# Optimization experiments

Measured on AMD Instinct MI355X. Metric: run time of the kernel, lower is better.

Reference implementation:

```python
import jax, jax.numpy as jnp
import numpy as np


def _make_cameras(key, B):
    """Well-conditioned c = [cam2world(16), intrinsics(9)] per batch."""
    k1, k2 = jax.random.split(key)
    # random rotation via Gram-Schmidt on a random 3x3
    A = jax.random.normal(k1, (B, 3, 3), dtype=jnp.float32)
    q0 = A[:, :, 0] / jnp.linalg.norm(A[:, :, 0], axis=-1, keepdims=True)
    v1 = A[:, :, 1] - jnp.sum(A[:, :, 1] * q0, -1, keepdims=True) * q0
    q1 = v1 / jnp.linalg.norm(v1, axis=-1, keepdims=True)
    q2 = jnp.cross(q0, q1)
    R = jnp.stack([q0, q1, q2], axis=-1)                      # [B,3,3]
    t = 2.7 * q2                                              # camera at radius 2.7 along view axis
    cam2world = jnp.zeros((B, 4, 4), jnp.float32)
    cam2world = cam2world.at[:, :3, :3].set(R)
    cam2world = cam2world.at[:, :3, 3].set(t)
    cam2world = cam2world.at[:, 3, 3].set(1.0)
    # EG3D-style normalized intrinsics: fx=fy=4.2647, cx=cy=0.5, sk=0
    intr = jnp.tile(jnp.array([[4.2647, 0.0, 0.5],
                               [0.0, 4.2647, 0.5],
                               [0.0, 0.0, 1.0]], jnp.float32), (B, 1, 1))
    return jnp.concatenate([cam2world.reshape(B, 16), intr.reshape(B, 9)], axis=1)


def setup_inputs() -> dict:
    key = jax.random.key(0)
    kc, kd, kp = jax.random.split(key, 3)
    B, R, M = 8, 64, 4096
    c = _make_cameras(kc, B)
    image_depth = 2.2 + 1.1 * jax.random.uniform(kd, (B, R * R, 1), dtype=jnp.float32)
    pc = 0.3 * jax.random.normal(kp, (B, M, 3), dtype=jnp.float32)
    return {"c": c, "image_depth": image_depth, "pc": pc, "resolution": R}


def _ray_sampler(cam2world, intrinsics, resolution):
    B = cam2world.shape[0]
    N = resolution * resolution
    fx = intrinsics[:, 0, 0][:, None]
    fy = intrinsics[:, 1, 1][:, None]
    cx = intrinsics[:, 0, 2][:, None]
    cy = intrinsics[:, 1, 2][:, None]
    sk = intrinsics[:, 0, 1][:, None]
    r = (jnp.arange(resolution, dtype=jnp.float32) + 0.5) / resolution
    gi, gj = jnp.meshgrid(r, r, indexing='ij')                # row, col
    x_cam = jnp.broadcast_to(gj.reshape(-1), (B, N))          # uv.flip(0): x is col coord
    y_cam = jnp.broadcast_to(gi.reshape(-1), (B, N))
    z_cam = jnp.ones((B, N), jnp.float32)
    x_lift = (x_cam - cx + cy * sk / fy - sk * y_cam / fy) / fx * z_cam
    y_lift = (y_cam - cy) / fy * z_cam
    cam_rel = jnp.stack([x_lift, y_lift, z_cam, jnp.ones_like(z_cam)], axis=-1)  # [B,N,4]
    world = jnp.einsum('bij,bnj->bni', cam2world, cam_rel)[..., :3]
    origins = cam2world[:, :3, 3]                              # [B,3]
    dirs = world - origins[:, None, :]
    dirs = dirs / jnp.linalg.norm(dirs, axis=-1, keepdims=True)
    ray_origins = jnp.broadcast_to(origins[:, None, :], dirs.shape)
    return ray_origins, dirs


def _chamfer(x, y):
    # squared-distance NN both directions; GEMM-form pairwise distances
    x2 = jnp.sum(x * x, axis=-1)                               # [B,N]
    y2 = jnp.sum(y * y, axis=-1)                               # [B,M]
    xy = jnp.einsum('bnd,bmd->bnm', x, y)                      # [B,N,M]
    d = x2[:, :, None] + y2[:, None, :] - 2.0 * xy
    return jnp.min(d, axis=2), jnp.min(d, axis=1)              # dist1 [B,N], dist2 [B,M]


def reference(c, image_depth, pc, resolution):
    B = c.shape[0]
    pc = pc[..., :3]
    depth = image_depth.reshape(B, -1, 1)
    cam2world = c[:, :16].reshape(-1, 4, 4)
    intr = c[:, 16:25].reshape(-1, 3, 3)
    ro, rd = _ray_sampler(cam2world, intr, resolution)
    pred_pos = depth * rd + ro                                  # [B,N,3]
    d0, d1 = _chamfer(pred_pos, pc)
    K = min(pred_pos.shape[1], pc.shape[1]) // 2
    d0s = jnp.sort(d0, axis=1)[:, :K]
    d1s = d0s  # NOTE: faithful to original code (loss_1_sorted is assigned from loss_0_sorted)
    loss0 = jnp.mean(d0s, axis=1)
    loss1 = jnp.mean(d1s, axis=1)
    return (loss0 + loss1).reshape(B, 1)
```

## Files before the change

### kernel.cpp

```cpp
#include <hip/hip_runtime.h>
#include <math.h>

#define FLT_BIG 3.0e38f
#define HIST_BINS 16384

typedef short short8 __attribute__((ext_vector_type(8)));
typedef float floatx16 __attribute__((ext_vector_type(16)));

union U4S8 { uint4 u; short8 s; };

static __device__ __forceinline__ unsigned int f2bf(float f) {
    unsigned int u = __float_as_uint(f);
    return (u + 0x7FFFu + ((u >> 16) & 1u)) >> 16;
}
static __device__ __forceinline__ float bf2f(unsigned int b) {
    return __uint_as_float(b << 16);
}

__global__ __launch_bounds__(256) void pack_frags_kernel(
    const float* __restrict__ pc,
    uint4* __restrict__ frags,
    int total)
{
    const int idx = blockIdx.x * 256 + threadIdx.x;
    if (idx >= total) return;
    const float x = pc[idx * 3 + 0];
    const float y = pc[idx * 3 + 1];
    const float z = pc[idx * 3 + 2];
    const float hq = 0.5f * (x * x + y * y + z * z);
    uint4 u;
    u.x = f2bf(x) | (f2bf(y) << 16);
    u.y = f2bf(z) | (f2bf(hq) << 16);
    u.z = 0x3F803F80u;
    u.w = 0u;
    frags[idx] = u;
}

__global__ __launch_bounds__(256, 4) void chamfer_mfma_kernel(
    const float* __restrict__ cparam,
    const float* __restrict__ depth,
    const uint4* __restrict__ frags,
    float* __restrict__ d0,
    int N, int M, int R)
{
    const int b    = blockIdx.y;
    const int tid  = threadIdx.x;
    const int lane = tid & 63;
    const int wv   = tid >> 6;
    const int row  = lane & 31;
    const int half = lane >> 5;

    __shared__ float smin[4][32];

    const float* cb = cparam + (size_t)b * 25;
    const float fx = cb[16], sk = cb[17], cx = cb[18];
    const float fy = cb[20], cy = cb[21];

    const int nbase = blockIdx.x * 32;
    const int n  = nbase + row;
    const int i0 = n / R;
    const int j0 = n - i0 * R;
    const float x_cam = (j0 + 0.5f) / (float)R;
    const float y_cam = (i0 + 0.5f) / (float)R;
    const float x_lift = (x_cam - cx + cy * sk / fy - sk * y_cam / fy) / fx;
    const float y_lift = (y_cam - cy) / fy;
    const float dxw = cb[0] * x_lift + cb[1] * y_lift + cb[2];
    const float dyw = cb[4] * x_lift + cb[5] * y_lift + cb[6];
    const float dzw = cb[8] * x_lift + cb[9] * y_lift + cb[10];
    const float inv = 1.0f / sqrtf(dxw * dxw + dyw * dyw + dzw * dzw);
    const float dep = depth[(size_t)b * N + n];
    const float px = cb[3]  + dep * dxw * inv;
    const float py = cb[7]  + dep * dyw * inv;
    const float pz = cb[11] + dep * dzw * inv;

    const float hp = 0.5f * (px * px + py * py + pz * pz);
    const unsigned int hp_hi = f2bf(hp);
    const unsigned int hp_lo = f2bf(hp - bf2f(hp_hi));

    U4S8 af;
    af.u = make_uint4(0u, 0u, 0u, 0u);
    if (half == 0) {
        af.u.x = f2bf(-px) | (f2bf(-py) << 16);
        af.u.y = f2bf(-pz) | (0x3F80u << 16);
        af.u.z = hp_hi | (hp_lo << 16);
    }
    const short8 afrag = af.s;
    const floatx16 zero16 = {0,0,0,0,0,0,0,0,0,0,0,0,0,0,0,0};

    float minsA[16], minsB[16];
    #pragma unroll
    for (int t = 0; t < 16; t++) { minsA[t] = FLT_BIG; minsB[t] = FLT_BIG; }

    const uint4* fb = frags + (size_t)b * M + (wv << 10);
    for (int f = 0; f < 32; f += 8) {
        uint4 bu[8];
        #pragma unroll
        for (int mm = 0; mm < 8; mm++)
            bu[mm] = fb[((f + mm) << 5) + row];
        #pragma unroll
        for (int mm = 0; mm < 8; mm++) {
            U4S8 bf; bf.u = bu[mm];
            floatx16 d = __builtin_amdgcn_mfma_f32_32x32x16_bf16(
                             afrag, bf.s, zero16, 0, 0, 0);
            if (mm & 1) {
                #pragma unroll
                for (int t = 0; t < 16; t++) minsB[t] = fminf(minsB[t], d[t]);
            } else {
                #pragma unroll
                for (int t = 0; t < 16; t++) minsA[t] = fminf(minsA[t], d[t]);
            }
        }
    }

    #pragma unroll
    for (int t = 0; t < 16; t++) {
        float v = fminf(minsA[t], minsB[t]);
        v = fminf(v, __shfl_xor(v, 1));
        v = fminf(v, __shfl_xor(v, 2));
        v = fminf(v, __shfl_xor(v, 4));
        v = fminf(v, __shfl_xor(v, 8));
        v = fminf(v, __shfl_xor(v, 16));
        minsA[t] = v;
    }
    if (row == 0) {
        #pragma unroll
        for (int t = 0; t < 16; t++)
            smin[wv][(t & 3) + 8 * (t >> 2) + 4 * half] = minsA[t];
    }
    __syncthreads();

    if (tid < 32) {
        const float v = fminf(fminf(smin[0][tid], smin[1][tid]),
                              fminf(smin[2][tid], smin[3][tid]));
        d0[(size_t)b * N + nbase + tid] = fmaxf(2.0f * v, 0.0f);
    }
}

__global__ __launch_bounds__(256, 1) void select_mean_kernel(
    const float* __restrict__ d0,
    float* __restrict__ out,
    int N, int K)
{
    const int b   = blockIdx.x;
    const int tid = threadIdx.x;

    extern __shared__ unsigned int hist[];
    __shared__ unsigned int spart[256];
    __shared__ unsigned int s_selbin, s_krem;
    __shared__ unsigned int subcnt[32];
    __shared__ float        subsum[32];
    __shared__ float        s_below;

    for (int t2 = tid; t2 < HIST_BINS; t2 += 256) hist[t2] = 0u;
    if (tid < 32) { subcnt[tid] = 0u; subsum[tid] = 0.0f; }
    if (tid == 0) s_below = 0.0f;
    __syncthreads();

    unsigned int key[16];
    #pragma unroll
    for (int t2 = 0; t2 < 16; t2++)
        key[t2] = __float_as_uint(d0[(size_t)b * N + t2 * 256 + tid]);
    #pragma unroll
    for (int t2 = 0; t2 < 16; t2++)
        atomicAdd(&hist[key[t2] >> 18], 1u);
    __syncthreads();

    unsigned int psum = 0u;
    #pragma unroll 8
    for (int i2 = 0; i2 < 64; i2++)
        psum += hist[(tid << 6) + ((i2 + tid) & 63)];
    spart[tid] = psum;
    __syncthreads();

    unsigned int cbef = 0u;
    for (int i2 = 0; i2 < tid; i2++) cbef += spart[i2];
    if (cbef < (unsigned int)K && (unsigned int)K <= cbef + psum) {
        unsigned int k2 = (unsigned int)K - cbef;
        unsigned int sel = 0u;
        for (int i2 = 0; i2 < 64; i2++) {
            unsigned int h = hist[(tid << 6) + i2];
            if (k2 <= h) { sel = (tid << 6) + i2; break; }
            k2 -= h;
        }
        s_selbin = sel;
        s_krem   = k2;
    }
    __syncthreads();

    const unsigned int selbin = s_selbin;
    float sumb = 0.0f;
    #pragma unroll
    for (int t2 = 0; t2 < 16; t2++) {
        const unsigned int bin = key[t2] >> 18;
        const float v = __uint_as_float(key[t2]);
        if (bin < selbin) sumb += v;
        if (bin == selbin) {
            const unsigned int sub = (key[t2] >> 13) & 31u;
            atomicAdd(&subcnt[sub], 1u);
            atomicAdd(&subsum[sub], v);
        }
    }
    atomicAdd(&s_below, sumb);
    __syncthreads();

    if (tid == 0) {
        unsigned int k2 = s_krem;
        float s = s_below;
        for (int i2 = 0; i2 < 32; i2++) {
            unsigned int h = subcnt[i2];
            if (k2 <= h) {
                s += (h ? (subsum[i2] * ((float)k2 / (float)h)) : 0.0f);
                break;
            }
            s += subsum[i2];
            k2 -= h;
        }
        out[b] = 2.0f * s / (float)K;
    }
}

extern "C" void kernel_launch(void* const* d_in, const int* in_sizes, int n_in,
                              void* d_out, int out_size, void* d_ws, size_t ws_size,
                              hipStream_t stream)
{
    const float* c   = (const float*)d_in[0];
    const float* dep = (const float*)d_in[1];
    const float* pc  = (const float*)d_in[2];
    float* out = (float*)d_out;

    const int B = in_sizes[0] / 25;
    const int N = in_sizes[1] / B;
    const int M = in_sizes[2] / (3 * B);
    int R = 1; while (R * R < N) R++;
    const int K = ((N < M) ? N : M) / 2;

    float* d0    = (float*)d_ws;
    uint4* frags = (uint4*)((char*)d_ws + (size_t)B * N * sizeof(float));

    const int total = B * M;
    hipLaunchKernelGGL(pack_frags_kernel, dim3((total + 255) / 256), dim3(256),
                       0, stream, pc, frags, total);

    dim3 gridA(N / 32, B);
    hipLaunchKernelGGL(chamfer_mfma_kernel, gridA, dim3(256), 0, stream,
                       c, dep, frags, d0, N, M, R);

    size_t ldsB = (size_t)HIST_BINS * sizeof(unsigned int);
    hipLaunchKernelGGL(select_mean_kernel, dim3(B), dim3(256), ldsB, stream,
                       d0, out, N, K);
}
```

Before: 82.62 us.

## Fuse point packing into chamfer kernel and widen select kernel to 1024 threads

Removes the separate pack kernel: the chamfer kernel now reads raw fp32 point coordinates and builds the bf16 MFMA B fragments in-register, including the half squared norm. The select/mean kernel moves to 1024 threads per batch, replacing the serial per-thread prefix loop over 256 partials with wave-level shuffle scans and a shuffle-reduced below-sum. This saves one launch and a round-trip through workspace. In exchange, every block now repacks every point (repeated conversion ALU work across N/32 blocks) and issues strided 12-byte loads in place of 16-byte vector loads.

```diff
diff --git a/kernel.cpp b/kernel.cpp
--- a/kernel.cpp
+++ b/kernel.cpp
@@ -17,29 +17,10 @@
     return __uint_as_float(b << 16);
 }
 
-__global__ __launch_bounds__(256) void pack_frags_kernel(
-    const float* __restrict__ pc,
-    uint4* __restrict__ frags,
-    int total)
-{
-    const int idx = blockIdx.x * 256 + threadIdx.x;
-    if (idx >= total) return;
-    const float x = pc[idx * 3 + 0];
-    const float y = pc[idx * 3 + 1];
-    const float z = pc[idx * 3 + 2];
-    const float hq = 0.5f * (x * x + y * y + z * z);
-    uint4 u;
-    u.x = f2bf(x) | (f2bf(y) << 16);
-    u.y = f2bf(z) | (f2bf(hq) << 16);
-    u.z = 0x3F803F80u;
-    u.w = 0u;
-    frags[idx] = u;
-}
-
 __global__ __launch_bounds__(256, 4) void chamfer_mfma_kernel(
     const float* __restrict__ cparam,
     const float* __restrict__ depth,
-    const uint4* __restrict__ frags,
+    const float* __restrict__ pc,
     float* __restrict__ d0,
     int N, int M, int R)
 {
@@ -91,15 +72,25 @@
     #pragma unroll
     for (int t = 0; t < 16; t++) { minsA[t] = FLT_BIG; minsB[t] = FLT_BIG; }
 
-    const uint4* fb = frags + (size_t)b * M + (wv << 10);
+    const float* qb = pc + ((size_t)b * M + ((size_t)wv << 10)) * 3;
     for (int f = 0; f < 32; f += 8) {
-        uint4 bu[8];
-        #pragma unroll
-        for (int mm = 0; mm < 8; mm++)
-            bu[mm] = fb[((f + mm) << 5) + row];
+        float qx[8], qy[8], qz[8];
         #pragma unroll
         for (int mm = 0; mm < 8; mm++) {
-            U4S8 bf; bf.u = bu[mm];
+            const int p = (((f + mm) << 5) + row) * 3;
+            qx[mm] = qb[p + 0];
+            qy[mm] = qb[p + 1];
+            qz[mm] = qb[p + 2];
+        }
+        #pragma unroll
+        for (int mm = 0; mm < 8; mm++) {
+            const float x = qx[mm], y = qy[mm], z = qz[mm];
+            const float hq = 0.5f * (x * x + y * y + z * z);
+            U4S8 bf;
+            bf.u.x = f2bf(x) | (f2bf(y) << 16);
+            bf.u.y = f2bf(z) | (f2bf(hq) << 16);
+            bf.u.z = 0x3F803F80u;
+            bf.u.w = 0u;
             floatx16 d = __builtin_amdgcn_mfma_f32_32x32x16_bf16(
                              afrag, bf.s, zero16, 0, 0, 0);
             if (mm & 1) {
@@ -136,50 +127,70 @@
     }
 }
 
-__global__ __launch_bounds__(256, 1) void select_mean_kernel(
+__global__ __launch_bounds__(1024, 1) void select_mean_kernel(
     const float* __restrict__ d0,
     float* __restrict__ out,
     int N, int K)
 {
-    const int b   = blockIdx.x;
-    const int tid = threadIdx.x;
+    const int b    = blockIdx.x;
+    const int tid  = threadIdx.x;
+    const int lane = tid & 63;
+    const int w    = tid >> 6;
 
     extern __shared__ unsigned int hist[];
-    __shared__ unsigned int spart[256];
+    __shared__ unsigned int wsums[16];
     __shared__ unsigned int s_selbin, s_krem;
     __shared__ unsigned int subcnt[32];
     __shared__ float        subsum[32];
     __shared__ float        s_below;
 
-    for (int t2 = tid; t2 < HIST_BINS; t2 += 256) hist[t2] = 0u;
+    #pragma unroll
+    for (int i = 0; i < 16; i++) hist[(i << 10) + tid] = 0u;
     if (tid < 32) { subcnt[tid] = 0u; subsum[tid] = 0.0f; }
     if (tid == 0) s_below = 0.0f;
     __syncthreads();
 
-    unsigned int key[16];
-    #pragma unroll
-    for (int t2 = 0; t2 < 16; t2++)
-        key[t2] = __float_as_uint(d0[(size_t)b * N + t2 * 256 + tid]);
-    #pragma unroll
-    for (int t2 = 0; t2 < 16; t2++)
-        atomicAdd(&hist[key[t2] >> 18], 1u);
+    unsigned int key[4];
+    #pragma unroll
+    for (int t = 0; t < 4; t++)
+        key[t] = __float_as_uint(d0[(size_t)b * N + (t << 10) + tid]);
+    #pragma unroll
+    for (int t = 0; t < 4; t++)
+        atomicAdd(&hist[key[t] >> 18], 1u);
     __syncthreads();
 
     unsigned int psum = 0u;
-    #pragma unroll 8
-    for (int i2 = 0; i2 < 64; i2++)
-        psum += hist[(tid << 6) + ((i2 + tid) & 63)];
-    spart[tid] = psum;
-    __syncthreads();
-
-    unsigned int cbef = 0u;
-    for (int i2 = 0; i2 < tid; i2++) cbef += spart[i2];
+    #pragma unroll
+    for (int i = 0; i < 16; i++)
+        psum += hist[(tid << 4) + ((i + tid) & 15)];
+
+    unsigned int inc = psum;
+    #pragma unroll
+    for (int dd = 1; dd < 64; dd <<= 1) {
+        unsigned int y = __shfl_up(inc, dd);
+        if (lane >= dd) inc += y;
+    }
+    if (lane == 63) wsums[w] = inc;
+    __syncthreads();
+    if (tid < 16) {
+        const unsigned int v = wsums[tid];
+        unsigned int in2 = v;
+        #pragma unroll
+        for (int dd = 1; dd < 16; dd <<= 1) {
+            unsigned int y = __shfl_up(in2, dd);
+            if ((int)tid >= dd) in2 += y;
+        }
+        wsums[tid] = in2 - v;
+    }
+    __syncthreads();
+    const unsigned int cbef = wsums[w] + (inc - psum);
+
     if (cbef < (unsigned int)K && (unsigned int)K <= cbef + psum) {
         unsigned int k2 = (unsigned int)K - cbef;
         unsigned int sel = 0u;
-        for (int i2 = 0; i2 < 64; i2++) {
-            unsigned int h = hist[(tid << 6) + i2];
-            if (k2 <= h) { sel = (tid << 6) + i2; break; }
+        for (int i = 0; i < 16; i++) {
+            unsigned int h = hist[(tid << 4) + i];
+            if (k2 <= h) { sel = (tid << 4) + i; break; }
             k2 -= h;
         }
         s_selbin = sel;
@@ -190,17 +201,19 @@
     const unsigned int selbin = s_selbin;
     float sumb = 0.0f;
     #pragma unroll
-    for (int t2 = 0; t2 < 16; t2++) {
-        const unsigned int bin = key[t2] >> 18;
-        const float v = __uint_as_float(key[t2]);
+    for (int t = 0; t < 4; t++) {
+        const unsigned int bin = key[t] >> 18;
+        const float v = __uint_as_float(key[t]);
         if (bin < selbin) sumb += v;
         if (bin == selbin) {
-            const unsigned int sub = (key[t2] >> 13) & 31u;
+            const unsigned int sub = (key[t] >> 13) & 31u;
             atomicAdd(&subcnt[sub], 1u);
             atomicAdd(&subsum[sub], v);
         }
     }
-    atomicAdd(&s_below, sumb);
+    #pragma unroll
+    for (int dd = 32; dd; dd >>= 1) sumb += __shfl_xor(sumb, dd);
+    if (lane == 0) atomicAdd(&s_below, sumb);
     __syncthreads();
 
     if (tid == 0) {
@@ -234,18 +247,13 @@
     int R = 1; while (R * R < N) R++;
     const int K = ((N < M) ? N : M) / 2;
 
-    float* d0    = (float*)d_ws;
-    uint4* frags = (uint4*)((char*)d_ws + (size_t)B * N * sizeof(float));
-
-    const int total = B * M;
-    hipLaunchKernelGGL(pack_frags_kernel, dim3((total + 255) / 256), dim3(256),
-                       0, stream, pc, frags, total);
+    float* d0 = (float*)d_ws;
 
     dim3 gridA(N / 32, B);
     hipLaunchKernelGGL(chamfer_mfma_kernel, gridA, dim3(256), 0, stream,
-                       c, dep, frags, d0, N, M, R);
+                       c, dep, pc, d0, N, M, R);
 
     size_t ldsB = (size_t)HIST_BINS * sizeof(unsigned int);
-    hipLaunchKernelGGL(select_mean_kernel, dim3(B), dim3(256), ldsB, stream,
+    hipLaunchKernelGGL(select_mean_kernel, dim3(B), dim3(1024), ldsB, stream,
                        d0, out, N, K);
 }
```

Result: faster. 78.79 us (-4.6%).
